# Optimization experiments

Measured on AMD Instinct MI355X. Metric: run time of the kernel, lower is better.

Reference implementation:

```python
import jax, jax.numpy as jnp
import numpy as np
import math

B_, CIN, CH, COUT, H_, W_ = 4, 96, 96, 96, 48, 48
DSTATE, DTRANK = 16, math.ceil(CH / 16)
DI = 2 * CH


def conv2d(x, w, b=None, groups=1):
    # x: NCHW, w: OIHW, 'same' padding for odd kernels
    p = (w.shape[-1] - 1) // 2
    y = jax.lax.conv_general_dilated(x, w, (1, 1), [(p, p), (p, p)],
                                     dimension_numbers=('NCHW', 'OIHW', 'NCHW'),
                                     feature_group_count=groups)
    return y if b is None else y + b[None, :, None, None]


def layernorm_last(x, g, b, eps=1e-5):
    mu = x.mean(-1, keepdims=True)
    v = jnp.mean((x - mu) ** 2, -1, keepdims=True)
    return (x - mu) * jax.lax.rsqrt(v + eps) * g + b


def selective_scan(u, delta, A, Bs, Cs, D):
    # u, delta: (B,K,Di,L); A: (K,Di,N); Bs, Cs: (B,K,N,L); D: (K,Di)
    dt = jnp.moveaxis(delta, -1, 0)  # (L,B,K,Di)
    ut = jnp.moveaxis(u, -1, 0)
    Bt = jnp.moveaxis(Bs, -1, 0)     # (L,B,K,N)
    Ct = jnp.moveaxis(Cs, -1, 0)
    N = A.shape[-1]

    def step(h, inp):
        d, uu, bb, cc = inp
        # h: (B,K,Di,N)
        h = h * jnp.exp(d[..., None] * A) + (d * uu)[..., None] * bb[:, :, None, :]
        y = jnp.einsum('bkdn,bkn->bkd', h, cc)
        return h, y

    step = jax.checkpoint(step)
    h0 = jnp.zeros(u.shape[:3] + (N,), u.dtype)
    _, ys = jax.lax.scan(step, h0, (dt, ut, Bt, Ct))
    return jnp.moveaxis(ys, 0, -1) + u * D[None, :, :, None]


def ss2d(x, in_w, cw, cb, xpw, dtw, dtb, A_log, Dp, ong, onb, ow):
    # x: (B,H,W,C) -> (B,H,W,C)
    B, H, W, C = x.shape
    Di = in_w.shape[0] // 2
    xi, z = jnp.split(x @ in_w.T, 2, -1)
    xc = jax.nn.silu(conv2d(jnp.transpose(xi, (0, 3, 1, 2)), cw, cb, groups=Di))
    L = H * W
    xf = xc.reshape(B, Di, L)
    xwh = jnp.transpose(xc, (0, 1, 3, 2)).reshape(B, Di, L)
    xh = jnp.stack([xf, xwh], 1)                      # (B,2,Di,L)
    xs = jnp.concatenate([xh, jnp.flip(xh, -1)], 1)   # (B,4,Di,L) 4-direction cross-scan
    xdbl = jnp.einsum('bkdl,kcd->bkcl', xs, xpw)
    R = dtw.shape[-1]
    N = A_log.shape[-1]
    dts, Bs, Cs = jnp.split(xdbl, [R, R + N], axis=2)
    delta = jax.nn.softplus(jnp.einsum('bkrl,kdr->bkdl', dts, dtw) + dtb[None, :, :, None])
    A = -jnp.exp(A_log.reshape(4, Di, N))
    oy = selective_scan(xs, delta, A, Bs, Cs, Dp.reshape(4, Di))  # (B,4,Di,L)
    inv = jnp.flip(oy[:, 2:4], -1)
    why = jnp.transpose(oy[:, 1].reshape(B, Di, W, H), (0, 1, 3, 2)).reshape(B, Di, L)
    invwhy = jnp.transpose(inv[:, 1].reshape(B, Di, W, H), (0, 1, 3, 2)).reshape(B, Di, L)
    y = oy[:, 0] + inv[:, 0] + why + invwhy           # (B,Di,L)
    y = layernorm_last(jnp.transpose(y, (0, 2, 1)).reshape(B, H, W, Di), ong, onb)
    return (y * jax.nn.silu(z)) @ ow.T


def crm(x, s1, s2, gw, gb, p1, p2):
    C = x.shape[1]
    uc = C // 2
    up = conv2d(x[:, :uc], s1)
    low = conv2d(x[:, uc:], s2)
    Y1 = conv2d(up, gw, gb, groups=2) + conv2d(up, p1)
    Y2 = jnp.concatenate([conv2d(low, p2), low], 1)
    out = jnp.concatenate([Y1, Y2], 1)                # (B,2C,H,W)
    out = jax.nn.softmax(out.mean((2, 3), keepdims=True), axis=1) * out
    o1, o2 = jnp.split(out, 2, 1)
    return o1 + o2


def _forward(x, conv1_w, conv1_b, bn_g, bn_b, lin_w, lin_b, dw1_w, dw1_b, dw2_w, dw2_b, ag1_w, ag1_b, ag2_w, ag2_b, ln_g, ln_b, sq1_w, sq2_w, gwc_w, gwc_b, pwc1_w, pwc2_w, fin_w, fin_b, ss_in_w, ss_conv_w, ss_conv_b, ss_xproj_w, ss_dt_w, ss_dt_b, ss_Alog, ss_D, ss_outn_g, ss_outn_b, ss_out_w):
    C = conv1_w.shape[0]
    # conv1x1 + BatchNorm(eval: running mean 0, var 1) + ReLU
    h = conv2d(x, conv1_w, conv1_b)
    h = jax.nn.relu(h * (bn_g * jax.lax.rsqrt(jnp.float32(1.0 + 1e-5)))[None, :, None, None] + bn_b[None, :, None, None])
    # token-wise linear over channels
    t = jnp.transpose(h, (0, 2, 3, 1)) @ lin_w.T + lin_b
    h = jnp.transpose(t, (0, 3, 1, 2))
    # branch 1: DWConv -> SiLU -> SS2D
    x1 = jax.nn.silu(conv2d(h, dw1_w, dw1_b, groups=C))
    x1 = ss2d(jnp.transpose(x1, (0, 2, 3, 1)), ss_in_w, ss_conv_w, ss_conv_b,
              ss_xproj_w, ss_dt_w, ss_dt_b, ss_Alog, ss_D, ss_outn_g, ss_outn_b, ss_out_w)
    x1 = jnp.transpose(x1, (0, 3, 1, 2))
    # branch 2: DWConv -> SiLU -> AttentionGate modulation
    x2 = jax.nn.silu(conv2d(h, dw2_w, dw2_b, groups=C))
    g = jax.nn.sigmoid(conv2d(jax.nn.relu(conv2d(x2, ag1_w, ag1_b)), ag2_w, ag2_b))
    y = x1 + x2 * g
    # per-pixel channel LayerNorm
    mu = y.mean(1, keepdims=True)
    v = jnp.mean((y - mu) ** 2, 1, keepdims=True)
    y = (y - mu) * jax.lax.rsqrt(v + 1e-5) * ln_g[None, :, None, None] + ln_b[None, :, None, None]
    y = crm(y, sq1_w, sq2_w, gwc_w, gwc_b, pwc1_w, pwc2_w)
    out = jnp.transpose(y, (0, 2, 3, 1)) @ fin_w.T + fin_b
    return jnp.transpose(out, (0, 3, 1, 2))


def setup_inputs():
    key = jax.random.key(0)

    def rnd(i, shape, s=0.02):
        return (jax.random.normal(jax.random.fold_in(key, i), shape) * s).astype(jnp.float32)

    CH2, N, R = CH // 2, DSTATE, DTRANK
    inp = dict(
        x=jax.random.normal(jax.random.fold_in(key, 0), (B_, CIN, H_, W_), jnp.float32),
        conv1_w=rnd(1, (CH, CIN, 1, 1)), conv1_b=jnp.zeros((CH,), jnp.float32),
        bn_g=jnp.ones((CH,), jnp.float32), bn_b=jnp.zeros((CH,), jnp.float32),
        lin_w=rnd(2, (CH, CH)), lin_b=jnp.zeros((CH,), jnp.float32),
        dw1_w=rnd(3, (CH, 1, 3, 3)), dw1_b=jnp.zeros((CH,), jnp.float32),
        dw2_w=rnd(4, (CH, 1, 3, 3)), dw2_b=jnp.zeros((CH,), jnp.float32),
        ag1_w=rnd(5, (CH2, CH, 1, 1)), ag1_b=jnp.zeros((CH2,), jnp.float32),
        ag2_w=rnd(6, (CH, CH2, 1, 1)), ag2_b=jnp.zeros((CH,), jnp.float32),
        ln_g=jnp.ones((CH,), jnp.float32), ln_b=jnp.zeros((CH,), jnp.float32),
        sq1_w=rnd(7, (CH // 4, CH2, 1, 1)), sq2_w=rnd(8, (CH // 4, CH2, 1, 1)),
        gwc_w=rnd(9, (CH, CH // 8, 3, 3)), gwc_b=jnp.zeros((CH,), jnp.float32),
        pwc1_w=rnd(10, (CH, CH // 4, 1, 1)), pwc2_w=rnd(11, (CH - CH // 4, CH // 4, 1, 1)),
        fin_w=rnd(12, (COUT, CH)), fin_b=jnp.zeros((COUT,), jnp.float32),
        ss_in_w=rnd(13, (2 * DI, CH)),
        ss_conv_w=rnd(14, (DI, 1, 3, 3)), ss_conv_b=jnp.zeros((DI,), jnp.float32),
        ss_xproj_w=rnd(15, (4, R + 2 * N, DI)),
        ss_dt_w=rnd(16, (4, DI, R), R ** -0.5),
    )
    dt = jnp.exp(jax.random.uniform(jax.random.fold_in(key, 17), (4, DI)) *
                 (math.log(0.1) - math.log(0.001)) + math.log(0.001))
    inp['ss_dt_b'] = (dt + jnp.log(-jnp.expm1(-dt))).astype(jnp.float32)
    inp['ss_Alog'] = jnp.tile(jnp.log(jnp.arange(1, DSTATE + 1, dtype=jnp.float32))[None, :], (4 * DI, 1))
    inp['ss_D'] = jnp.ones((4 * DI,), jnp.float32)
    inp['ss_outn_g'] = jnp.ones((DI,), jnp.float32)
    inp['ss_outn_b'] = jnp.zeros((DI,), jnp.float32)
    inp['ss_out_w'] = rnd(18, (CH, DI))
    return inp


def reference(x, conv1_w, conv1_b, bn_g, bn_b, lin_w, lin_b, dw1_w, dw1_b, dw2_w, dw2_b, ag1_w, ag1_b, ag2_w, ag2_b, ln_g, ln_b, sq1_w, sq2_w, gwc_w, gwc_b, pwc1_w, pwc2_w, fin_w, fin_b, ss_in_w, ss_conv_w, ss_conv_b, ss_xproj_w, ss_dt_w, ss_dt_b, ss_Alog, ss_D, ss_outn_g, ss_outn_b, ss_out_w):
    return _forward(x, conv1_w, conv1_b, bn_g, bn_b, lin_w, lin_b, dw1_w, dw1_b, dw2_w, dw2_b, ag1_w, ag1_b, ag2_w, ag2_b, ln_g, ln_b, sq1_w, sq2_w, gwc_w, gwc_b, pwc1_w, pwc2_w, fin_w, fin_b, ss_in_w, ss_conv_w, ss_conv_b, ss_xproj_w, ss_dt_w, ss_dt_b, ss_Alog, ss_D, ss_outn_g, ss_outn_b, ss_out_w)
```

## Files before the change

kernel.cpp:

```cpp
#include <hip/hip_runtime.h>
#include <hip/hip_bf16.h>

#define Bn   4
#define CHn  96
#define Hh   48
#define Ww   48
#define Ll   2304
#define Pp   9216
#define DIn  192
#define Nn   16
#define Rr   6
#define Sseg   32
#define SEGL   72
#define NCH     9
#define HSPLIT 884736

__device__ inline float siluf(float x){ return x / (1.0f + __expf(-x)); }
__device__ inline float sigmf(float x){ return 1.0f / (1.0f + __expf(-x)); }

__device__ inline int pix_of(int k, int l){
  if (k == 0) return l;
  if (k == 1) return (l % 48) * 48 + l / 48;
  if (k == 2) return Ll - 1 - l;
  int lr = Ll - 1 - l; return (lr % 48) * 48 + lr / 48;
}
__device__ inline int l_of(int k, int p){
  if (k == 0) return p;
  if (k == 1) return (p % 48) * 48 + p / 48;
  if (k == 2) return Ll - 1 - p;
  return Ll - 1 - ((p % 48) * 48 + p / 48);
}

__device__ inline float4* hptr(float* lo, float* hi, size_t idx){
  return (float4*)(idx < HSPLIT ? lo + idx : hi + (idx - HSPLIT));
}

struct TArgs {
  const float* s[14];
  float* d[14];
  int rows[14];
  int cols[14];
};
__global__ void k_tr(TArgs a){
  int id = blockIdx.y;
  int n = a.rows[id] * a.cols[id];
  int t = blockIdx.x * blockDim.x + threadIdx.x;
  if (t < n){
    int r = t / a.cols[id];
    int c = t - r * a.cols[id];
    a.d[id][c * a.rows[id] + r] = a.s[id][t];
  }
}

__global__ __launch_bounds__(256) void k_pre(const float* __restrict__ x, const float* __restrict__ w1T, const float* __restrict__ b1,
                      const float* __restrict__ bng, const float* __restrict__ bnb,
                      const float* __restrict__ linT, const float* __restrict__ lb,
                      float* __restrict__ hlin){
  __shared__ float xv[16][97];
  __shared__ float hv[16][97];
  int tid = threadIdx.x;
  int m = tid >> 4, t = tid & 15;
  int p0 = blockIdx.x * 16;
  int b = p0 / Ll; int pp0 = p0 - b * Ll;
  #pragma unroll
  for (int it = 0; it < 6; ++it){
    int e = it * 256 + tid; int c = e >> 4; int mm = e & 15;
    xv[mm][c] = x[((size_t)(b * CHn + c)) * Ll + pp0 + mm];
  }
  __syncthreads();
  float acc[6];
  #pragma unroll
  for (int j = 0; j < 6; ++j) acc[j] = 0.f;
  for (int i = 0; i < CHn; ++i){
    float xval = xv[m][i];
    #pragma unroll
    for (int j = 0; j < 6; ++j)
      acc[j] = fmaf(w1T[i * CHn + t + 16 * j], xval, acc[j]);
  }
  #pragma unroll
  for (int j = 0; j < 6; ++j){
    int c = t + 16 * j;
    float s = bng[c] * rsqrtf(1.0f + 1e-5f);
    hv[m][c] = fmaxf((acc[j] + b1[c]) * s + bnb[c], 0.f);
  }
  __syncthreads();
  float a2[6];
  #pragma unroll
  for (int j = 0; j < 6; ++j) a2[j] = lb[t + 16 * j];
  for (int i = 0; i < CHn; ++i){
    float hval = hv[m][i];
    #pragma unroll
    for (int j = 0; j < 6; ++j)
      a2[j] = fmaf(linT[i * CHn + t + 16 * j], hval, a2[j]);
  }
  int p = p0 + m;
  #pragma unroll
  for (int j = 0; j < 6; ++j)
    hlin[(size_t)p * CHn + t + 16 * j] = a2[j];
}

__global__ void k_dw(const float* __restrict__ hlin,
                     const float* __restrict__ dw1w, const float* __restrict__ dw1b,
                     const float* __restrict__ dw2w, const float* __restrict__ dw2b,
                     float* __restrict__ x1pre, float* __restrict__ x2){
  int t = blockIdx.x * 256 + threadIdx.x;
  if (t >= Pp * CHn) return;
  int c = t % CHn; int p = t / CHn; int b = p / Ll; int pp = p - b * Ll;
  int r = pp / Ww; int cx = pp - r * Ww;
  float a1 = dw1b[c], a2 = dw2b[c];
  for (int dy = -1; dy <= 1; ++dy){
    int ny = r + dy; if ((unsigned)ny >= Hh) continue;
    for (int dx = -1; dx <= 1; ++dx){
      int nx = cx + dx; if ((unsigned)nx >= Ww) continue;
      float v = hlin[(size_t)((b * Ll) + ny * Ww + nx) * CHn + c];
      int wi = c * 9 + (dy + 1) * 3 + (dx + 1);
      a1 = fmaf(dw1w[wi], v, a1);
      a2 = fmaf(dw2w[wi], v, a2);
    }
  }
  x1pre[t] = siluf(a1);
  x2[t]   = siluf(a2);
}

__global__ __launch_bounds__(256) void k_gate(const float* __restrict__ x2,
                       const float* __restrict__ ag1T, const float* __restrict__ ag1b,
                       const float* __restrict__ ag2T, const float* __restrict__ ag2b,
                       float* __restrict__ x2g){
  __shared__ float xv[16][97];
  __shared__ float rv[16][49];
  int tid = threadIdx.x;
  int m = tid >> 4, t = tid & 15;
  int p0 = blockIdx.x * 16;
  #pragma unroll
  for (int it = 0; it < 6; ++it){
    int e = it * 256 + tid; int mm = e / 96; int c = e - mm * 96;
    xv[mm][c] = x2[(size_t)(p0 + mm) * CHn + c];
  }
  __syncthreads();
  float a[3];
  #pragma unroll
  for (int jj = 0; jj < 3; ++jj) a[jj] = ag1b[t + 16 * jj];
  for (int i = 0; i < CHn; ++i){
    float xval = xv[m][i];
    #pragma unroll
    for (int jj = 0; jj < 3; ++jj)
      a[jj] = fmaf(ag1T[i * 48 + t + 16 * jj], xval, a[jj]);
  }
  #pragma unroll
  for (int jj = 0; jj < 3; ++jj) rv[m][t + 16 * jj] = fmaxf(a[jj], 0.f);
  __syncthreads();
  float a2[6];
  #pragma unroll
  for (int j = 0; j < 6; ++j) a2[j] = ag2b[t + 16 * j];
  for (int i = 0; i < 48; ++i){
    float rval = rv[m][i];
    #pragma unroll
    for (int j = 0; j < 6; ++j)
      a2[j] = fmaf(ag2T[i * CHn + t + 16 * j], rval, a2[j]);
  }
  int p = p0 + m;
  #pragma unroll
  for (int j = 0; j < 6; ++j){
    int c = t + 16 * j;
    x2g[(size_t)p * CHn + c] = xv[m][c] * sigmf(a2[j]);
  }
}

__global__ __launch_bounds__(256) void k_ssin(const float* __restrict__ x1pre, const float* __restrict__ inT,
                                              float* __restrict__ xi, float* __restrict__ z){
  __shared__ float Xs[32][17];
  __shared__ float Wsh[32][128];
  int tid = threadIdx.x;
  int mt = blockIdx.x % 576; int nt = blockIdx.x / 576;
  int p0 = mt * 16, n0 = nt * 128;
  int tx = tid & 15, ty = tid >> 4;
  float acc[8];
  #pragma unroll
  for (int j = 0; j < 8; ++j) acc[j] = 0.f;
  for (int kc = 0; kc < 96; kc += 32){
    #pragma unroll
    for (int it = 0; it < 2; ++it){
      int e = it * 256 + tid; int dd = e & 31; int m = e >> 5;
      Xs[dd][m] = x1pre[(size_t)(p0 + m) * CHn + kc + dd];
    }
    #pragma unroll
    for (int it = 0; it < 16; ++it){
      int e = it * 256 + tid; int n = e & 127; int dd = e >> 7;
      Wsh[dd][n] = inT[(size_t)(kc + dd) * 384 + n0 + n];
    }
    __syncthreads();
    #pragma unroll
    for (int dd = 0; dd < 32; ++dd){
      float xv = Xs[dd][ty];
      #pragma unroll
      for (int j = 0; j < 8; ++j)
        acc[j] = fmaf(xv, Wsh[dd][tx + 16 * j], acc[j]);
    }
    __syncthreads();
  }
  int p = p0 + ty;
  #pragma unroll
  for (int j = 0; j < 8; ++j){
    int n = n0 + tx + 16 * j;
    float v = acc[j];
    if (n < 192) xi[(size_t)p * DIn + n] = v;
    else         z [(size_t)p * DIn + (n - 192)] = v;
  }
}

__global__ void k_ssdw(const float* __restrict__ xi, const float* __restrict__ scw,
                       const float* __restrict__ scb, float* __restrict__ xc){
  int t = blockIdx.x * 256 + threadIdx.x;
  if (t >= Pp * DIn) return;
  int d = t % DIn; int p = t / DIn; int b = p / Ll; int pp = p - b * Ll;
  int r = pp / Ww; int cx = pp - r * Ww;
  float a = scb[d];
  for (int dy = -1; dy <= 1; ++dy){
    int ny = r + dy; if ((unsigned)ny >= Hh) continue;
    for (int dx = -1; dx <= 1; ++dx){
      int nx = cx + dx; if ((unsigned)nx >= Ww) continue;
      float v = xi[(size_t)((b * Ll) + ny * Ww + nx) * DIn + d];
      a = fmaf(scw[d * 9 + (dy + 1) * 3 + (dx + 1)], v, a);
    }
  }
  xc[t] = siluf(a);
}

__global__ __launch_bounds__(256) void k_xproj(const float* __restrict__ xc,
    const float* __restrict__ xpwT, float* __restrict__ part){
  __shared__ float Xs[32][33];
  __shared__ float Wsh[32][160];
  int tid = threadIdx.x;
  int mt = blockIdx.x / 6; int kc = (blockIdx.x - mt * 6) * 32;
  int p0g = mt * 32;
  int tx = tid & 15, ty = tid >> 4;
  const float* xbase = xc + (size_t)p0g * DIn + kc;
  #pragma unroll
  for (int it = 0; it < 4; ++it){
    int e = it * 256 + tid; int dd = e & 31; int m = e >> 5;
    Xs[dd][m] = xbase[(size_t)m * DIn + dd];
  }
  #pragma unroll
  for (int it = 0; it < 20; ++it){
    int e = it * 256 + tid; int dd = e / 160; int n = e - dd * 160;
    Wsh[dd][n] = (n < 152) ? xpwT[(size_t)(kc + dd) * 152 + n] : 0.f;
  }
  __syncthreads();
  float a0[4], a1[4], b0[4], b1[4], c0[2], c1[2];
  #pragma unroll
  for (int i = 0; i < 4; ++i){ a0[i] = a1[i] = b0[i] = b1[i] = 0.f; }
  c0[0] = c0[1] = c1[0] = c1[1] = 0.f;
  #pragma unroll
  for (int dd = 0; dd < 32; ++dd){
    float x0 = Xs[dd][ty];
    float x1 = Xs[dd][ty + 16];
    float4 wa = *(const float4*)&Wsh[dd][tx * 4];
    float4 wb = *(const float4*)&Wsh[dd][64 + tx * 4];
    float2 wc = *(const float2*)&Wsh[dd][128 + tx * 2];
    a0[0] = fmaf(x0, wa.x, a0[0]); a0[1] = fmaf(x0, wa.y, a0[1]);
    a0[2] = fmaf(x0, wa.z, a0[2]); a0[3] = fmaf(x0, wa.w, a0[3]);
    a1[0] = fmaf(x1, wa.x, a1[0]); a1[1] = fmaf(x1, wa.y, a1[1]);
    a1[2] = fmaf(x1, wa.z, a1[2]); a1[3] = fmaf(x1, wa.w, a1[3]);
    b0[0] = fmaf(x0, wb.x, b0[0]); b0[1] = fmaf(x0, wb.y, b0[1]);
    b0[2] = fmaf(x0, wb.z, b0[2]); b0[3] = fmaf(x0, wb.w, b0[3]);
    b1[0] = fmaf(x1, wb.x, b1[0]); b1[1] = fmaf(x1, wb.y, b1[1]);
    b1[2] = fmaf(x1, wb.z, b1[2]); b1[3] = fmaf(x1, wb.w, b1[3]);
    c0[0] = fmaf(x0, wc.x, c0[0]); c0[1] = fmaf(x0, wc.y, c0[1]);
    c1[0] = fmaf(x1, wc.x, c1[0]); c1[1] = fmaf(x1, wc.y, c1[1]);
  }
  float* pb0 = part + ((size_t)blockIdx.x * 32 + ty) * 152;
  float* pb1 = part + ((size_t)blockIdx.x * 32 + ty + 16) * 152;
  #pragma unroll
  for (int i = 0; i < 4; ++i){
    pb0[tx * 4 + i] = a0[i];      pb1[tx * 4 + i] = a1[i];
    pb0[64 + tx * 4 + i] = b0[i]; pb1[64 + tx * 4 + i] = b1[i];
  }
  #pragma unroll
  for (int i = 0; i < 2; ++i){
    int n = 128 + tx * 2 + i;
    if (n < 152){ pb0[n] = c0[i]; pb1[n] = c1[i]; }
  }
}

__global__ void k_xred(const float* __restrict__ part, float* __restrict__ bc,
                       float* __restrict__ dtsG){
  int t = blockIdx.x * 256 + threadIdx.x;
  if (t >= Pp * 152) return;
  int p = t / 152, n = t - p * 152;
  int mt = p >> 5, m = p & 31;
  const float* pb = part + ((size_t)(mt * 6) * 32 + m) * 152 + n;
  float s = 0.f;
  #pragma unroll
  for (int kc = 0; kc < 6; ++kc) s += pb[(size_t)kc * 32 * 152];
  int b = p / Ll; int pp = p - b * Ll;
  int k = n / 38, jj = n - k * 38;
  int l = l_of(k, pp);
  if (jj < 6) dtsG[((size_t)((b * 4 + k) * Ll + l)) * 6 + jj] = s;
  else        bc [((size_t)((b * 4 + k) * Ll + l)) * 32 + (jj - 6)] = s;
}

__global__ void k_pack(const float* __restrict__ dtsG, const float* __restrict__ dtwT,
                       const float* __restrict__ dtb, const float* __restrict__ xc,
                       float* __restrict__ packed){
  int t = blockIdx.x * 256 + threadIdx.x;
  if (t >= 36864 * DIn) return;
  int d = t % DIn; int row = t / DIn;
  int bk = row / Ll; int l = row - bk * Ll;
  int k = bk & 3; int b = bk >> 2;
  const float* ds = dtsG + (size_t)row * 6;
  float a = dtb[k * DIn + d];
  #pragma unroll
  for (int r = 0; r < 6; ++r)
    a = fmaf(dtwT[r * 768 + k * DIn + d], ds[r], a);
  float dt = fmaxf(a, 0.f) + __logf(1.0f + __expf(-fabsf(a)));
  int pix = pix_of(k, l);
  float u = xc[((size_t)(b * Ll) + pix) * DIn + d];
  int unit = bk * 12 + (d >> 4);
  size_t base = ((size_t)unit * Ll + l) * 32 + (d & 15);
  packed[base]      = dt;
  packed[base + 16] = dt * u;
}


__global__ __launch_bounds__(64) void k_scanA(const float* __restrict__ packed, const float* __restrict__ bc,
                                              const float* __restrict__ Alog,
                                              float* __restrict__ hend, float* __restrict__ dtsum){
  int blk = blockIdx.x; int unit = blk >> 5; int seg = blk & 31;
  int g = unit % 12; int bk = unit / 12; int k = bk & 3;
  int lane = threadIdx.x; int ch = lane >> 2; int ns = lane & 3; int nb = ns * 4;
  int d = g * 16 + ch;
  const int arow = (k * DIn + d) * 16 + nb;
  float A0 = -__expf(Alog[arow + 0]);
  float A1 = -__expf(Alog[arow + 1]);
  float A2 = -__expf(Alog[arow + 2]);
  float A3 = -__expf(Alog[arow + 3]);
  float h0 = 0.f, h1 = 0.f, h2 = 0.f, h3 = 0.f, dacc = 0.f;

  const int l0 = seg * SEGL;
  const float* pbase = packed + ((size_t)unit * Ll + l0) * 32;
  const float* bbase = bc + ((size_t)(bk * Ll) + l0) * 32;

  __shared__ float pl[256];
  __shared__ float blA[128];

  float4 pn = *(const float4*)(pbase + lane * 4);
  float4 bn;
  if (lane < 32) bn = *(const float4*)(bbase + (size_t)(lane >> 2) * 32 + (lane & 3) * 4);
  *(float4*)&pl[lane * 4] = pn;
  if (lane < 32) *(float4*)&blA[lane * 4] = bn;
  __syncthreads();

  for (int cc = 0; cc < NCH; ++cc){
    bool more = (cc + 1 < NCH);
    if (more){
      pn = *(const float4*)(pbase + (cc + 1) * 256 + lane * 4);
      if (lane < 32) bn = *(const float4*)(bbase + (size_t)((cc + 1) * 8 + (lane >> 2)) * 32 + (lane & 3) * 4);
    }
    #pragma unroll
    for (int lp = 0; lp < 8; ++lp){
      float dt = pl[lp * 32 + ch];
      float du = pl[lp * 32 + 16 + ch];
      float4 Bv = *(const float4*)&blA[lp * 16 + nb];
      dacc += dt;
      h0 = fmaf(h0, __expf(dt * A0), du * Bv.x);
      h1 = fmaf(h1, __expf(dt * A1), du * Bv.y);
      h2 = fmaf(h2, __expf(dt * A2), du * Bv.z);
      h3 = fmaf(h3, __expf(dt * A3), du * Bv.w);
    }
    __syncthreads();
    if (more){
      *(float4*)&pl[lane * 4] = pn;
      if (lane < 32) *(float4*)&blA[lane * 4] = bn;
    }
    __syncthreads();
  }
  size_t sb = (size_t)unit * Sseg + seg;
  *(float4*)&hend[sb * 256 + lane * 4] = make_float4(h0, h1, h2, h3);
  if (ns == 0) dtsum[sb * 16 + ch] = dacc;
}

__global__ __launch_bounds__(64) void k_comb(const float* __restrict__ Alog, const float* __restrict__ hend,
                                             const float* __restrict__ dtsum,
                                             float* __restrict__ hlo, float* __restrict__ hhi){
  int unit = blockIdx.x; int g = unit % 12; int bk = unit / 12; int k = bk & 3;
  int lane = threadIdx.x; int ch = lane >> 2; int ns = lane & 3; int nb = ns * 4;
  int d = g * 16 + ch;
  const int arow = (k * DIn + d) * 16 + nb;
  float A0 = -__expf(Alog[arow + 0]);
  float A1 = -__expf(Alog[arow + 1]);
  float A2 = -__expf(Alog[arow + 2]);
  float A3 = -__expf(Alog[arow + 3]);
  float h0 = 0.f, h1 = 0.f, h2 = 0.f, h3 = 0.f;
  for (int s = 0; s < Sseg; ++s){
    size_t sb = (size_t)unit * Sseg + s;
    *hptr(hlo, hhi, sb * 256 + lane * 4) = make_float4(h0, h1, h2, h3);
    float dsv = dtsum[sb * 16 + ch];
    float4 he = *(const float4*)&hend[sb * 256 + lane * 4];
    h0 = fmaf(h0, __expf(A0 * dsv), he.x);
    h1 = fmaf(h1, __expf(A1 * dsv), he.y);
    h2 = fmaf(h2, __expf(A2 * dsv), he.z);
    h3 = fmaf(h3, __expf(A3 * dsv), he.w);
  }
}

__global__ __launch_bounds__(64) void k_scanB(const float* __restrict__ packed, const float* __restrict__ bc,
                                              const float* __restrict__ Alog,
                                              float* __restrict__ hlo, float* __restrict__ hhi,
                                              float* __restrict__ ysum){
  int blk = blockIdx.x; int unit = blk >> 5; int seg = blk & 31;
  int g = unit % 12; int bk = unit / 12; int k = bk & 3; int b = bk >> 2;
  int lane = threadIdx.x; int ch = lane >> 2; int ns = lane & 3; int nb = ns * 4;
  int d = g * 16 + ch;
  const int arow = (k * DIn + d) * 16 + nb;
  float A0 = -__expf(Alog[arow + 0]);
  float A1 = -__expf(Alog[arow + 1]);
  float A2 = -__expf(Alog[arow + 2]);
  float A3 = -__expf(Alog[arow + 3]);
  size_t sb = (size_t)unit * Sseg + seg;
  float4 hi = *hptr(hlo, hhi, sb * 256 + lane * 4);
  float h0 = hi.x, h1 = hi.y, h2 = hi.z, h3 = hi.w;

  const int l0 = seg * SEGL;
  const float* pbase = packed + ((size_t)unit * Ll + l0) * 32;
  const float* bbase = bc + ((size_t)(bk * Ll) + l0) * 32;
  float* ybase = ysum + (size_t)(b * Ll) * DIn + d;

  __shared__ float pl[256];
  __shared__ float bl[256];

  float4 pn = *(const float4*)(pbase + lane * 4);
  float4 bn = *(const float4*)(bbase + lane * 4);
  *(float4*)&pl[lane * 4] = pn;
  *(float4*)&bl[lane * 4] = bn;
  __syncthreads();

  for (int cc = 0; cc < NCH; ++cc){
    bool more = (cc + 1 < NCH);
    if (more){
      pn = *(const float4*)(pbase + (cc + 1) * 256 + lane * 4);
      bn = *(const float4*)(bbase + (cc + 1) * 256 + lane * 4);
    }
    #pragma unroll
    for (int lp = 0; lp < 8; ++lp){
      float dt = pl[lp * 32 + ch];
      float du = pl[lp * 32 + 16 + ch];
      float4 Bv = *(const float4*)&bl[lp * 32 + nb];
      float4 Cv = *(const float4*)&bl[lp * 32 + 16 + nb];
      h0 = fmaf(h0, __expf(dt * A0), du * Bv.x);
      h1 = fmaf(h1, __expf(dt * A1), du * Bv.y);
      h2 = fmaf(h2, __expf(dt * A2), du * Bv.z);
      h3 = fmaf(h3, __expf(dt * A3), du * Bv.w);
      float yp = fmaf(h0, Cv.x, fmaf(h1, Cv.y, fmaf(h2, Cv.z, h3 * Cv.w)));
      yp += __shfl_xor(yp, 1);
      yp += __shfl_xor(yp, 2);
      if (ns == 0){
        int l = l0 + cc * 8 + lp;
        int pix = pix_of(k, l);
        atomicAdd(ybase + (size_t)pix * DIn, yp);
      }
    }
    __syncthreads();
    if (more){
      *(float4*)&pl[lane * 4] = pn;
      *(float4*)&bl[lane * 4] = bn;
    }
    __syncthreads();
  }
}

__device__ inline float block_sum_192(float* red, int d, float v){
  red[d] = v; __syncthreads();
  if (d < 96) red[d] += red[d + 96]; __syncthreads();
  if (d < 48) red[d] += red[d + 48]; __syncthreads();
  if (d < 24) red[d] += red[d + 24]; __syncthreads();
  if (d < 12) red[d] += red[d + 12]; __syncthreads();
  if (d < 6)  red[d] += red[d + 6];  __syncthreads();
  float tot = red[0] + red[1] + red[2] + red[3] + red[4] + red[5];
  __syncthreads();
  return tot;
}

__global__ __launch_bounds__(256) void k_lngate(const float* __restrict__ ysum, const float* __restrict__ xc,
                        const float* __restrict__ z, const float* __restrict__ Dp,
                        const float* __restrict__ ong, const float* __restrict__ onb,
                        float* __restrict__ ygb){
  int tid = threadIdx.x;
  int w = tid >> 6;
  int l = tid & 63;
  int p = blockIdx.x * 4 + w;
  const float* yrow = ysum + (size_t)p * DIn;
  const float* urow = xc   + (size_t)p * DIn;
  const float* zrow = z    + (size_t)p * DIn;
  float yv[3]; float s1 = 0.f;
  #pragma unroll
  for (int j = 0; j < 3; ++j){
    int d = l + 64 * j;
    float Ds = Dp[d] + Dp[192 + d] + Dp[384 + d] + Dp[576 + d];
    float v = fmaf(urow[d], Ds, yrow[d]);
    yv[j] = v; s1 += v;
  }
  #pragma unroll
  for (int mk = 1; mk < 64; mk <<= 1) s1 += __shfl_xor(s1, mk, 64);
  float mu = s1 * (1.f / 192.f);
  float s2 = 0.f;
  #pragma unroll
  for (int j = 0; j < 3; ++j){ float dv = yv[j] - mu; s2 += dv * dv; }
  #pragma unroll
  for (int mk = 1; mk < 64; mk <<= 1) s2 += __shfl_xor(s2, mk, 64);
  float rstd = rsqrtf(s2 * (1.f / 192.f) + 1e-5f);
  #pragma unroll
  for (int j = 0; j < 3; ++j){
    int d = l + 64 * j;
    float yn = (yv[j] - mu) * rstd * ong[d] + onb[d];
    float zv = zrow[d];
    ygb[(size_t)p * DIn + d] = yn * (zv * sigmf(zv));
  }
}

__global__ __launch_bounds__(256) void k_oproj(const float* __restrict__ ygb, const float* __restrict__ owT,
                       float* __restrict__ part2){
  __shared__ float Xs[32][17];
  __shared__ float Wsh[32][97];
  int tid = threadIdx.x;
  int mt = blockIdx.x >> 1; int kh = (blockIdx.x & 1) * 96;
  int p0 = mt * 16;
  int tx = tid & 15, ty = tid >> 4;
  float acc[6];
  #pragma unroll
  for (int jj = 0; jj < 6; ++jj) acc[jj] = 0.f;
  for (int kc = 0; kc < 96; kc += 32){
    #pragma unroll
    for (int it = 0; it < 2; ++it){
      int e = it * 256 + tid; int dd = e & 31; int m = e >> 5;
      Xs[dd][m] = ygb[(size_t)(p0 + m) * DIn + kh + kc + dd];
    }
    #pragma unroll
    for (int it = 0; it < 12; ++it){
      int e = it * 256 + tid; int dd = e / 96; int n = e - dd * 96;
      Wsh[dd][n] = owT[(size_t)(kh + kc + dd) * 96 + n];
    }
    __syncthreads();
    #pragma unroll
    for (int dd = 0; dd < 32; ++dd){
      float xv = Xs[dd][ty];
      #pragma unroll
      for (int jj = 0; jj < 6; ++jj)
        acc[jj] = fmaf(xv, Wsh[dd][tx + 16 * jj], acc[jj]);
    }
    __syncthreads();
  }
  float* pb = part2 + ((size_t)blockIdx.x * 16 + ty) * 96;
  #pragma unroll
  for (int jj = 0; jj < 6; ++jj)
    pb[tx + 16 * jj] = acc[jj];
}

__global__ __launch_bounds__(256) void k_finc(const float* __restrict__ part2, const float* __restrict__ x2g,
                      const float* __restrict__ lng, const float* __restrict__ lnb,
                      const float* __restrict__ sq1T, const float* __restrict__ sq2T,
                      float* __restrict__ ul){
  __shared__ float crs_s[16 * 104];
  __shared__ float sqs[2304];
  int tid = threadIdx.x;
  int m = tid >> 4, t = tid & 15;
  int mt = blockIdx.x;
  int p = mt * 16 + m;
  #pragma unroll
  for (int it = 0; it < 5; ++it){
    int e = it * 256 + tid;
    if (e < 1152) sqs[e] = sq1T[e];
  }
  #pragma unroll
  for (int it = 0; it < 5; ++it){
    int e = it * 256 + tid;
    if (e < 1152) sqs[1152 + e] = sq2T[e];
  }
  const float* pa = part2 + ((size_t)(mt * 2)     * 16 + m) * 96;
  const float* pbp = part2 + ((size_t)(mt * 2 + 1) * 16 + m) * 96;
  float sv[6]; float s3 = 0.f;
  #pragma unroll
  for (int jj = 0; jj < 6; ++jj){
    int c = t + 16 * jj;
    float v = pa[c] + pbp[c] + x2g[(size_t)p * CHn + c];
    sv[jj] = v; s3 += v;
  }
  #pragma unroll
  for (int mk = 1; mk < 16; mk <<= 1) s3 += __shfl_xor(s3, mk, 16);
  float mu2 = s3 * (1.f / 96.f);
  float s4 = 0.f;
  #pragma unroll
  for (int jj = 0; jj < 6; ++jj){ float dv = sv[jj] - mu2; s4 += dv * dv; }
  #pragma unroll
  for (int mk = 1; mk < 16; mk <<= 1) s4 += __shfl_xor(s4, mk, 16);
  float rstd2 = rsqrtf(s4 * (1.f / 96.f) + 1e-5f);
  #pragma unroll
  for (int jj = 0; jj < 6; ++jj){
    int c = t + 16 * jj;
    crs_s[m * 104 + c] = (sv[jj] - mu2) * rstd2 * lng[c] + lnb[c];
  }
  __syncthreads();
  const float* cr = &crs_s[m * 104];
  #pragma unroll
  for (int jj = 0; jj < 3; ++jj){
    int o = t + 16 * jj;
    float a = 0.f;
    if (o < 24){
      for (int i = 0; i < 48; ++i) a = fmaf(sqs[i * 24 + o], cr[i], a);
    } else {
      int oo = o - 24;
      for (int i = 0; i < 48; ++i) a = fmaf(sqs[1152 + i * 24 + oo], cr[48 + i], a);
    }
    ul[(size_t)p * 48 + o] = a;
  }
}

__global__ __launch_bounds__(256) void k_y(const float* __restrict__ ul, const float* __restrict__ gwcT,
                    const float* __restrict__ gwcb, const float* __restrict__ pwc1T,
                    const float* __restrict__ pwc2T, float* __restrict__ Ybig){
  __shared__ float uls[3 * 18 * 48];
  int tid = threadIdx.x;
  int m = tid >> 4, t = tid & 15;
  int blk = blockIdx.x;
  int b = blk / 144; int rem = blk - b * 144;
  int r = rem / 3; int chunk = rem - r * 3;
  int cx0 = chunk * 16;
  for (int e = tid; e < 3 * 18 * 48; e += 256){
    int ch = e % 48; int rc = e / 48;
    int col = rc % 18; int row = rc / 18;
    int gr = r - 1 + row; int gc = cx0 - 1 + col;
    float v = 0.f;
    if ((unsigned)gr < Hh && (unsigned)gc < Ww)
      v = ul[((size_t)(b * Ll + gr * Ww + gc)) * 48 + ch];
    uls[e] = v;
  }
  __syncthreads();
  int p = b * Ll + r * Ww + cx0 + m;
  const float* u1 = &uls[(1 * 18 + m + 1) * 48];
  float* yout = Ybig + (size_t)p * 192;
  #pragma unroll 1
  for (int j = 0; j < 6; ++j){
    int oc = t + 16 * j;
    int grp = oc / 48;
    float acc = gwcb[oc];
    #pragma unroll 1
    for (int k9 = 0; k9 < 9; ++k9){
      int dy = k9 / 3; int dx = k9 - dy * 3;
      const float* un = &uls[((dy * 18) + m + dx) * 48 + grp * 12];
      const float* wrow = gwcT + k9 * 96 + oc;
      #pragma unroll
      for (int i = 0; i < 12; ++i)
        acc = fmaf(wrow[i * 864], un[i], acc);
    }
    #pragma unroll
    for (int i = 0; i < 24; ++i) acc = fmaf(pwc1T[i * 96 + oc], u1[i], acc);
    yout[oc] = acc;
  }
  #pragma unroll 1
  for (int j = 6; j < 12; ++j){
    int oc = t + 16 * j;
    float acc;
    if (oc < 168){
      int o2 = oc - 96; acc = 0.f;
      #pragma unroll
      for (int i = 0; i < 24; ++i) acc = fmaf(pwc2T[i * 72 + o2], u1[24 + i], acc);
    } else {
      acc = u1[24 + oc - 168];
    }
    yout[oc] = acc;
  }
}

__global__ void k_csum(const float* __restrict__ Ybig, float* __restrict__ csum_p){
  int b = blockIdx.x / 144; int ch = blockIdx.x - b * 144;
  int t = threadIdx.x;
  if (t >= 192) return;
  float acc = 0.f;
  const float* base = Ybig + (size_t)(b * Ll + ch * 16) * 192 + t;
  #pragma unroll
  for (int i = 0; i < 16; ++i) acc += base[(size_t)i * 192];
  csum_p[(size_t)blockIdx.x * 192 + t] = acc;
}

__global__ void k_softmax(const float* __restrict__ csum_p, float* __restrict__ wsm){
  int b = blockIdx.x; int t = threadIdx.x;
  __shared__ float red[192];
  float m = 0.f;
  for (int cc = 0; cc < 144; ++cc) m += csum_p[(size_t)(b * 144 + cc) * 192 + t];
  m *= (1.f / 2304.f);
  red[t] = m; __syncthreads();
  if (t < 96) red[t] = fmaxf(red[t], red[t + 96]); __syncthreads();
  if (t < 48) red[t] = fmaxf(red[t], red[t + 48]); __syncthreads();
  if (t < 24) red[t] = fmaxf(red[t], red[t + 24]); __syncthreads();
  if (t < 12) red[t] = fmaxf(red[t], red[t + 12]); __syncthreads();
  if (t < 6)  red[t] = fmaxf(red[t], red[t + 6]);  __syncthreads();
  float mx = fmaxf(fmaxf(fmaxf(red[0], red[1]), fmaxf(red[2], red[3])), fmaxf(red[4], red[5]));
  __syncthreads();
  float e = __expf(m - mx);
  float s = block_sum_192(red, t, e);
  wsm[b * 192 + t] = e / s;
}

__global__ __launch_bounds__(256) void k_final(const float* __restrict__ Ybig, const float* __restrict__ wsm,
                        const float* __restrict__ finT, const float* __restrict__ finb,
                        float* __restrict__ out){
  __shared__ float ys[16][193];
  __shared__ float ov[16][97];
  __shared__ float wv[192];
  int tid = threadIdx.x;
  int m = tid >> 4, t = tid & 15;
  int p0 = blockIdx.x * 16;
  int b = p0 / Ll; int pp0 = p0 - b * Ll;
  if (tid < 192) wv[tid] = wsm[b * 192 + tid];
  #pragma unroll
  for (int it = 0; it < 12; ++it){
    int e = it * 256 + tid; int mm = e / 192; int c = e - mm * 192;
    ys[mm][c] = Ybig[(size_t)(p0 + mm) * 192 + c];
  }
  __syncthreads();
  #pragma unroll
  for (int j = 0; j < 6; ++j){
    int c = t + 16 * j;
    ov[m][c] = wv[c] * ys[m][c] + wv[96 + c] * ys[m][96 + c];
  }
  __syncthreads();
  float res[6];
  #pragma unroll
  for (int j = 0; j < 6; ++j) res[j] = finb[t + 16 * j];
  for (int i = 0; i < 96; ++i){
    float oval = ov[m][i];
    #pragma unroll
    for (int j = 0; j < 6; ++j)
      res[j] = fmaf(finT[i * 96 + t + 16 * j], oval, res[j]);
  }
  #pragma unroll
  for (int j = 0; j < 6; ++j) ys[m][t + 16 * j] = res[j];
  __syncthreads();
  #pragma unroll
  for (int it = 0; it < 6; ++it){
    int e = it * 256 + tid; int c = e >> 4; int mm = e & 15;
    out[((size_t)(b * CHn + c)) * Ll + pp0 + mm] = ys[mm][c];
  }
}

extern "C" void kernel_launch(void* const* d_in, const int* in_sizes, int n_in,
                              void* d_out, int out_size, void* d_ws, size_t ws_size,
                              hipStream_t stream) {
  const float* x     = (const float*)d_in[0];
  const float* w1    = (const float*)d_in[1];
  const float* b1    = (const float*)d_in[2];
  const float* bng   = (const float*)d_in[3];
  const float* bnb   = (const float*)d_in[4];
  const float* linw  = (const float*)d_in[5];
  const float* linb  = (const float*)d_in[6];
  const float* dw1w  = (const float*)d_in[7];
  const float* dw1b  = (const float*)d_in[8];
  const float* dw2w  = (const float*)d_in[9];
  const float* dw2b  = (const float*)d_in[10];
  const float* ag1w  = (const float*)d_in[11];
  const float* ag1b  = (const float*)d_in[12];
  const float* ag2w  = (const float*)d_in[13];
  const float* ag2b  = (const float*)d_in[14];
  const float* lng   = (const float*)d_in[15];
  const float* lnb   = (const float*)d_in[16];
  const float* sq1w  = (const float*)d_in[17];
  const float* sq2w  = (const float*)d_in[18];
  const float* gwcw  = (const float*)d_in[19];
  const float* gwcb  = (const float*)d_in[20];
  const float* pwc1w = (const float*)d_in[21];
  const float* pwc2w = (const float*)d_in[22];
  const float* finw  = (const float*)d_in[23];
  const float* finb  = (const float*)d_in[24];
  const float* inw   = (const float*)d_in[25];
  const float* scw   = (const float*)d_in[26];
  const float* scb   = (const float*)d_in[27];
  const float* xpw   = (const float*)d_in[28];
  const float* dtw   = (const float*)d_in[29];
  const float* dtb   = (const float*)d_in[30];
  const float* Alog  = (const float*)d_in[31];
  const float* Dp    = (const float*)d_in[32];
  const float* ong   = (const float*)d_in[33];
  const float* onb   = (const float*)d_in[34];
  const float* oww   = (const float*)d_in[35];

  float* ws = (float*)d_ws;
  float* hlin   = ws + 0;
  float* dtsum  = ws + 442368;
  float* x1pre  = ws + 884736;
  float* x2     = ws + 1769472;
  float* x2g    = ws + 2654208;
  float* xibuf  = ws + 3538944;
  float* zbuf   = ws + 5308416;
  float* xcbuf  = ws + 7077888;
  float* packed = ws + 8847360;
  float* bcbuf  = ws + 23003136;
  float* ysum   = ws + 24182784;
  float* wT     = ws + 25952256;

  float* dtsG    = x2;
  float* hend    = xibuf;
  float* hinitlo = x1pre;
  float* hinithi = x2;
  float* ulb     = hlin;
  float* Ybig    = xibuf;
  float* csum_p  = x1pre;
  float* wsmb    = x1pre + 110592;
  float* part    = packed;
  float* ygb     = packed;
  float* part2   = packed + 1769472;

  float* w1T   = wT + 0;
  float* linT  = wT + 9216;
  float* ag1T  = wT + 18432;
  float* ag2T  = wT + 23040;
  float* inT   = wT + 27648;
  float* owT   = wT + 64512;
  float* pwc1T = wT + 82944;
  float* pwc2T = wT + 85248;
  float* finT  = wT + 86976;
  float* sq1T  = wT + 96192;
  float* sq2T  = wT + 97344;
  float* gwcT  = wT + 98496;
  float* dtwT  = wT + 108864;
  float* xpwT  = wT + 113472;

  TArgs ta;
  const float* srcs[14] = {w1, linw, ag1w, ag2w, inw, oww, pwc1w, pwc2w, finw, sq1w, sq2w, gwcw, dtw, xpw};
  float* dsts[14]       = {w1T, linT, ag1T, ag2T, inT, owT, pwc1T, pwc2T, finT, sq1T, sq2T, gwcT, dtwT, xpwT};
  int rows[14] = {96, 96, 48, 96, 384, 96, 96, 72, 96, 24, 24, 96, 768, 152};
  int cols[14] = {96, 96, 96, 48, 96, 192, 24, 24, 96, 48, 48, 108, 6, 192};
  for (int i = 0; i < 14; ++i){ ta.s[i] = srcs[i]; ta.d[i] = dsts[i]; ta.rows[i] = rows[i]; ta.cols[i] = cols[i]; }

  k_tr<<<dim3(144, 14), 256, 0, stream>>>(ta);
  k_pre<<<576, 256, 0, stream>>>(x, w1T, b1, bng, bnb, linT, linb, hlin);
  k_dw<<<(Pp * CHn) / 256, 256, 0, stream>>>(hlin, dw1w, dw1b, dw2w, dw2b, x1pre, x2);
  k_gate<<<576, 256, 0, stream>>>(x2, ag1T, ag1b, ag2T, ag2b, x2g);
  k_ssin<<<576 * 3, 256, 0, stream>>>(x1pre, inT, xibuf, zbuf);
  k_ssdw<<<(Pp * DIn) / 256, 256, 0, stream>>>(xibuf, scw, scb, xcbuf);
  k_xproj<<<288 * 6, 256, 0, stream>>>(xcbuf, xpwT, part);
  k_xred<<<(Pp * 152 + 255) / 256, 256, 0, stream>>>(part, bcbuf, dtsG);
  k_pack<<<(36864 * DIn) / 256, 256, 0, stream>>>(dtsG, dtwT, dtb, xcbuf, packed);
  hipMemsetAsync(ysum, 0, (size_t)1769472 * 4, stream);
  k_scanA<<<192 * Sseg, 64, 0, stream>>>(packed, bcbuf, Alog, hend, dtsum);
  k_comb<<<192, 64, 0, stream>>>(Alog, hend, dtsum, hinitlo, hinithi);
  k_scanB<<<192 * Sseg, 64, 0, stream>>>(packed, bcbuf, Alog, hinitlo, hinithi, ysum);
  k_lngate<<<2304, 256, 0, stream>>>(ysum, xcbuf, zbuf, Dp, ong, onb, ygb);
  k_oproj<<<1152, 256, 0, stream>>>(ygb, owT, part2);
  k_finc<<<576, 256, 0, stream>>>(part2, x2g, lng, lnb, sq1T, sq2T, ulb);
  k_y<<<576, 256, 0, stream>>>(ulb, gwcT, gwcb, pwc1T, pwc2T, Ybig);
  k_csum<<<576, 256, 0, stream>>>(Ybig, csum_p);
  k_softmax<<<4, 192, 0, stream>>>(csum_p, wsmb);
  k_final<<<576, 256, 0, stream>>>(Ybig, wsmb, finT, finb, (float*)d_out);
}
```

Measured before the change: 323.6 us.

## Vectorize GEMM smem reads and write transposed xc copy for pack gathers

The ssin and oproj GEMM inner loops now read weights from shared memory as float4/float2 with contiguous per-thread column groups, and the ssin output is written with float4 stores. The depthwise conv kernel also writes a transposed copy of xc (W-major order), so k_pack can read u for the column-scan directions with a direct index instead of a strided gather through pix_of. This adds an extra full-size write of xc and a new workspace region, and the column layout change alters the shared-memory bank access pattern.

```diff
diff --git a/kernel.cpp b/kernel.cpp
--- a/kernel.cpp
+++ b/kernel.cpp
@@ -174,9 +174,9 @@
   int mt = blockIdx.x % 576; int nt = blockIdx.x / 576;
   int p0 = mt * 16, n0 = nt * 128;
   int tx = tid & 15, ty = tid >> 4;
-  float acc[8];
-  #pragma unroll
-  for (int j = 0; j < 8; ++j) acc[j] = 0.f;
+  float accA[4], accB[4];
+  #pragma unroll
+  for (int j = 0; j < 4; ++j){ accA[j] = 0.f; accB[j] = 0.f; }
   for (int kc = 0; kc < 96; kc += 32){
     #pragma unroll
     for (int it = 0; it < 2; ++it){
@@ -192,24 +192,29 @@
     #pragma unroll
     for (int dd = 0; dd < 32; ++dd){
       float xv = Xs[dd][ty];
-      #pragma unroll
-      for (int j = 0; j < 8; ++j)
-        acc[j] = fmaf(xv, Wsh[dd][tx + 16 * j], acc[j]);
+      float4 wa = *(const float4*)&Wsh[dd][tx * 4];
+      float4 wb = *(const float4*)&Wsh[dd][64 + tx * 4];
+      accA[0] = fmaf(xv, wa.x, accA[0]); accA[1] = fmaf(xv, wa.y, accA[1]);
+      accA[2] = fmaf(xv, wa.z, accA[2]); accA[3] = fmaf(xv, wa.w, accA[3]);
+      accB[0] = fmaf(xv, wb.x, accB[0]); accB[1] = fmaf(xv, wb.y, accB[1]);
+      accB[2] = fmaf(xv, wb.z, accB[2]); accB[3] = fmaf(xv, wb.w, accB[3]);
     }
     __syncthreads();
   }
   int p = p0 + ty;
-  #pragma unroll
-  for (int j = 0; j < 8; ++j){
-    int n = n0 + tx + 16 * j;
-    float v = acc[j];
-    if (n < 192) xi[(size_t)p * DIn + n] = v;
-    else         z [(size_t)p * DIn + (n - 192)] = v;
-  }
+  int na = n0 + tx * 4;
+  int nb2 = n0 + 64 + tx * 4;
+  float4 va = make_float4(accA[0], accA[1], accA[2], accA[3]);
+  float4 vb = make_float4(accB[0], accB[1], accB[2], accB[3]);
+  if (na < 192) *(float4*)&xi[(size_t)p * DIn + na] = va;
+  else          *(float4*)&z [(size_t)p * DIn + (na - 192)] = va;
+  if (nb2 < 192) *(float4*)&xi[(size_t)p * DIn + nb2] = vb;
+  else           *(float4*)&z [(size_t)p * DIn + (nb2 - 192)] = vb;
 }
 
 __global__ void k_ssdw(const float* __restrict__ xi, const float* __restrict__ scw,
-                       const float* __restrict__ scb, float* __restrict__ xc){
+                       const float* __restrict__ scb, float* __restrict__ xc,
+                       float* __restrict__ xcT){
   int t = blockIdx.x * 256 + threadIdx.x;
   if (t >= Pp * DIn) return;
   int d = t % DIn; int p = t / DIn; int b = p / Ll; int pp = p - b * Ll;
@@ -223,7 +228,10 @@
       a = fmaf(scw[d * 9 + (dy + 1) * 3 + (dx + 1)], v, a);
     }
   }
-  xc[t] = siluf(a);
+  float val = siluf(a);
+  xc[t] = val;
+  int lt = cx * 48 + r;
+  xcT[((size_t)(b * Ll) + lt) * DIn + d] = val;
 }
 
 __global__ __launch_bounds__(256) void k_xproj(const float* __restrict__ xc,
@@ -301,7 +309,7 @@
 
 __global__ void k_pack(const float* __restrict__ dtsG, const float* __restrict__ dtwT,
                        const float* __restrict__ dtb, const float* __restrict__ xc,
-                       float* __restrict__ packed){
+                       const float* __restrict__ xcT, float* __restrict__ packed){
   int t = blockIdx.x * 256 + threadIdx.x;
   if (t >= 36864 * DIn) return;
   int d = t % DIn; int row = t / DIn;
@@ -313,8 +321,9 @@
   for (int r = 0; r < 6; ++r)
     a = fmaf(dtwT[r * 768 + k * DIn + d], ds[r], a);
   float dt = fmaxf(a, 0.f) + __logf(1.0f + __expf(-fabsf(a)));
-  int pix = pix_of(k, l);
-  float u = xc[((size_t)(b * Ll) + pix) * DIn + d];
+  int lr = (k & 2) ? (Ll - 1 - l) : l;
+  const float* src = (k & 1) ? xcT : xc;
+  float u = src[((size_t)(b * Ll) + lr) * DIn + d];
   int unit = bk * 12 + (d >> 4);
   size_t base = ((size_t)unit * Ll + l) * 32 + (d & 15);
   packed[base]      = dt;
@@ -520,14 +529,13 @@
 __global__ __launch_bounds__(256) void k_oproj(const float* __restrict__ ygb, const float* __restrict__ owT,
                        float* __restrict__ part2){
   __shared__ float Xs[32][17];
-  __shared__ float Wsh[32][97];
+  __shared__ float Wsh[32][100];
   int tid = threadIdx.x;
   int mt = blockIdx.x >> 1; int kh = (blockIdx.x & 1) * 96;
   int p0 = mt * 16;
   int tx = tid & 15, ty = tid >> 4;
-  float acc[6];
-  #pragma unroll
-  for (int jj = 0; jj < 6; ++jj) acc[jj] = 0.f;
+  float aA[4], aB[2];
+  aA[0] = aA[1] = aA[2] = aA[3] = 0.f; aB[0] = aB[1] = 0.f;
   for (int kc = 0; kc < 96; kc += 32){
     #pragma unroll
     for (int it = 0; it < 2; ++it){
@@ -543,16 +551,19 @@
     #pragma unroll
     for (int dd = 0; dd < 32; ++dd){
       float xv = Xs[dd][ty];
-      #pragma unroll
-      for (int jj = 0; jj < 6; ++jj)
-        acc[jj] = fmaf(xv, Wsh[dd][tx + 16 * jj], acc[jj]);
+      float4 wa = *(const float4*)&Wsh[dd][tx * 4];
+      float2 wb = *(const float2*)&Wsh[dd][64 + tx * 2];
+      aA[0] = fmaf(xv, wa.x, aA[0]); aA[1] = fmaf(xv, wa.y, aA[1]);
+      aA[2] = fmaf(xv, wa.z, aA[2]); aA[3] = fmaf(xv, wa.w, aA[3]);
+      aB[0] = fmaf(xv, wb.x, aB[0]); aB[1] = fmaf(xv, wb.y, aB[1]);
     }
     __syncthreads();
   }
   float* pb = part2 + ((size_t)blockIdx.x * 16 + ty) * 96;
   #pragma unroll
-  for (int jj = 0; jj < 6; ++jj)
-    pb[tx + 16 * jj] = acc[jj];
+  for (int i = 0; i < 4; ++i) pb[tx * 4 + i] = aA[i];
+  #pragma unroll
+  for (int i = 0; i < 2; ++i) pb[64 + tx * 2 + i] = aB[i];
 }
 
 __global__ __launch_bounds__(256) void k_finc(const float* __restrict__ part2, const float* __restrict__ x2g,
@@ -795,6 +806,7 @@
   float* bcbuf  = ws + 23003136;
   float* ysum   = ws + 24182784;
   float* wT     = ws + 25952256;
+  float* xcTbuf = ws + 26094912;
 
   float* dtsG    = x2;
   float* hend    = xibuf;
@@ -835,10 +847,10 @@
   k_dw<<<(Pp * CHn) / 256, 256, 0, stream>>>(hlin, dw1w, dw1b, dw2w, dw2b, x1pre, x2);
   k_gate<<<576, 256, 0, stream>>>(x2, ag1T, ag1b, ag2T, ag2b, x2g);
   k_ssin<<<576 * 3, 256, 0, stream>>>(x1pre, inT, xibuf, zbuf);
-  k_ssdw<<<(Pp * DIn) / 256, 256, 0, stream>>>(xibuf, scw, scb, xcbuf);
+  k_ssdw<<<(Pp * DIn) / 256, 256, 0, stream>>>(xibuf, scw, scb, xcbuf, xcTbuf);
   k_xproj<<<288 * 6, 256, 0, stream>>>(xcbuf, xpwT, part);
   k_xred<<<(Pp * 152 + 255) / 256, 256, 0, stream>>>(part, bcbuf, dtsG);
-  k_pack<<<(36864 * DIn) / 256, 256, 0, stream>>>(dtsG, dtwT, dtb, xcbuf, packed);
+  k_pack<<<(36864 * DIn) / 256, 256, 0, stream>>>(dtsG, dtwT, dtb, xcbuf, xcTbuf, packed);
   hipMemsetAsync(ysum, 0, (size_t)1769472 * 4, stream);
   k_scanA<<<192 * Sseg, 64, 0, stream>>>(packed, bcbuf, Alog, hend, dtsum);
   k_comb<<<192, 64, 0, stream>>>(Alog, hend, dtsum, hinitlo, hinithi);
```

New measurement: 314.7 us. -2.8%, faster.
